# Performance work log

Hardware: AMD Instinct MI355X
Metric: run time of the kernel (lower is better)

## Reference

```python
import jax, jax.numpy as jnp
import numpy as np

N, IN_DIM, HID, OUT = 8192, 512, 256, 64
NEG_INF = -9e15


def setup_inputs() -> dict:
    key = jax.random.key(0)
    ks = jax.random.split(key, 7)
    X = jax.random.normal(ks[0], (N, IN_DIM), dtype=jnp.float32)
    A = jax.random.randint(ks[1], (N, N), 0, 2, dtype=jnp.int32)
    # fc1 (Linear): kaiming-uniform-ish init, exact dist irrelevant for correctness
    W1 = jax.random.normal(ks[2], (IN_DIM, HID), dtype=jnp.float32) / np.sqrt(IN_DIM)
    b1 = jnp.zeros((HID,), dtype=jnp.float32)
    # attention vector a: xavier_uniform(gain=1.414) on shape (2*HID, 1)
    lim = 1.414 * np.sqrt(6.0 / (2 * HID + 1))
    a = jax.random.uniform(ks[3], (2 * HID, 1), minval=-lim, maxval=lim, dtype=jnp.float32)
    Omega = jax.random.normal(ks[4], (HID, OUT), dtype=jnp.float32) * np.sqrt(2.0 / (HID + OUT))
    beta = jnp.zeros((OUT,), dtype=jnp.float32)
    return {"X": X, "A": A, "W1": W1, "b1": b1, "a": a, "Omega": Omega, "beta": beta}


def reference(X, A, W1, b1, a, Omega, beta):
    H1 = X @ W1 + b1                      # [N, HID]
    # score(i,j) = leakyrelu(a[:HID].H1_i + a[HID:].H1_j) -- computed via broadcast,
    # avoiding the O(N^2 * 2*HID) concat the torch code materializes.
    a1 = a[:HID, 0]                       # [HID]
    a2 = a[HID:, 0]                       # [HID]
    e = jax.nn.leaky_relu((H1 @ a1)[:, None] + (H1 @ a2)[None, :], negative_slope=0.2)  # [N, N]
    e = jnp.where(A > 0, e, NEG_INF)
    attention = jax.nn.softmax(e, axis=1)  # dropout_rate=0.0 -> identity
    H2 = attention @ H1                    # [N, HID]
    return jax.nn.sigmoid(H2 @ Omega + beta)  # [N, OUT]
```

## Files before the change

### kernel.cpp

```cpp
#include <hip/hip_runtime.h>
#include <hip/hip_bf16.h>


typedef float f32x4 __attribute__((ext_vector_type(4)));
typedef short s16x8 __attribute__((ext_vector_type(8)));

#define NN 8192
#define INDIM 512
#define HIDD 256
#define OUTD 64

static __device__ __forceinline__ short f2bf(float x) {
    __hip_bfloat16 h = __float2bfloat16(x);
    return __builtin_bit_cast(short, h);
}

static __device__ __forceinline__ void split_bf(float x, short& hi, short& lo) {
    short h = f2bf(x);
    unsigned int hb = ((unsigned int)(unsigned short)h) << 16;
    float hf = __builtin_bit_cast(float, hb);
    hi = h;
    lo = f2bf(x - hf);
}

__global__ void k_splitW1(const float* __restrict__ W1,
                          short* __restrict__ W1Thi, short* __restrict__ W1Tlo) {
    int t = blockIdx.x * 256 + threadIdx.x;
    int n = t >> 9;
    int k = t & 511;
    float x = W1[k * 256 + n];
    short hi, lo; split_bf(x, hi, lo);
    W1Thi[t] = hi;
    W1Tlo[t] = lo;
}

__global__ void __launch_bounds__(256, 2)
k_h1(const float* __restrict__ X, const short* __restrict__ W1Thi,
     const short* __restrict__ W1Tlo, const float* __restrict__ b1,
     const float* __restrict__ avec, unsigned short* __restrict__ H1TB,
     float* __restrict__ alw, float* __restrict__ bew, float* __restrict__ uvw) {
    __shared__ float s1p[4][16];
    __shared__ float s2p[4][16];
    const int tid = threadIdx.x;
    const int wn = tid >> 6, lane = tid & 63;
    const int q = lane >> 4, m16 = lane & 15;
    const int i0 = blockIdx.x * 16;
    const int irow = i0 + m16;

    f32x4 zero4 = {0.f, 0.f, 0.f, 0.f};
    f32x4 acc[4];
#pragma unroll
    for (int nt = 0; nt < 4; ++nt) acc[nt] = zero4;

    const float* Xrow = X + (size_t)irow * INDIM;
    for (int kk = 0; kk < INDIM; kk += 32) {
        const int k0 = kk + q * 8;
        float4 xa = *(const float4*)(Xrow + k0);
        float4 xb = *(const float4*)(Xrow + k0 + 4);
        float xs[8] = {xa.x, xa.y, xa.z, xa.w, xb.x, xb.y, xb.z, xb.w};
        s16x8 ahi, alo;
#pragma unroll
        for (int j = 0; j < 8; ++j) { short h, l; split_bf(xs[j], h, l); ahi[j] = h; alo[j] = l; }
#pragma unroll
        for (int nt = 0; nt < 4; ++nt) {
            const int n = wn * 64 + nt * 16 + m16;
            s16x8 bhi = *(const s16x8*)(W1Thi + n * INDIM + k0);
            s16x8 blo = *(const s16x8*)(W1Tlo + n * INDIM + k0);
            acc[nt] = __builtin_amdgcn_mfma_f32_16x16x32_bf16(ahi, bhi, acc[nt], 0, 0, 0);
            acc[nt] = __builtin_amdgcn_mfma_f32_16x16x32_bf16(ahi, blo, acc[nt], 0, 0, 0);
            acc[nt] = __builtin_amdgcn_mfma_f32_16x16x32_bf16(alo, bhi, acc[nt], 0, 0, 0);
        }
    }

    float p1[4] = {0.f, 0.f, 0.f, 0.f};
    float p2[4] = {0.f, 0.f, 0.f, 0.f};
    const int rowbase = i0 + q * 4;
    const int chunk = rowbase >> 5, win = rowbase & 31;
#pragma unroll
    for (int nt = 0; nt < 4; ++nt) {
        const int col = wn * 64 + nt * 16 + m16;
        const float b1v = b1[col];
        const float a1v = avec[col];
        const float a2v = avec[HIDD + col];
        float v0 = acc[nt][0] + b1v;
        float v1 = acc[nt][1] + b1v;
        float v2 = acc[nt][2] + b1v;
        float v3 = acc[nt][3] + b1v;
        ushort4 us;
        us.x = (unsigned short)f2bf(v0);
        us.y = (unsigned short)f2bf(v1);
        us.z = (unsigned short)f2bf(v2);
        us.w = (unsigned short)f2bf(v3);
        *(ushort4*)(H1TB + (size_t)chunk * 8192 + col * 32 + win) = us;
        p1[0] += v0 * a1v; p1[1] += v1 * a1v; p1[2] += v2 * a1v; p1[3] += v3 * a1v;
        p2[0] += v0 * a2v; p2[1] += v1 * a2v; p2[2] += v2 * a2v; p2[3] += v3 * a2v;
    }
#pragma unroll
    for (int off = 1; off < 16; off <<= 1) {
#pragma unroll
        for (int r = 0; r < 4; ++r) {
            p1[r] += __shfl_xor(p1[r], off);
            p2[r] += __shfl_xor(p2[r], off);
        }
    }
    if (m16 == 0) {
#pragma unroll
        for (int r = 0; r < 4; ++r) {
            s1p[wn][q * 4 + r] = p1[r];
            s2p[wn][q * 4 + r] = p2[r];
        }
    }
    __syncthreads();
    if (tid < 16) {
        const int i = i0 + tid;
        float s1 = s1p[0][tid] + s1p[1][tid] + s1p[2][tid] + s1p[3][tid];
        float s2 = s2p[0][tid] + s2p[1][tid] + s2p[2][tid] + s2p[3][tid];
        alw[i] = expf(s1);
        bew[i] = expf(0.2f * s1);
        uvw[2 * i]     = expf(s2);
        uvw[2 * i + 1] = expf(0.2f * s2);
    }
}

__global__ void __launch_bounds__(256, 4)
k_attn(const int* __restrict__ A, const unsigned short* __restrict__ H1TB,
       const float* __restrict__ alw, const float* __restrict__ bew,
       const float* __restrict__ uvw,
       float* __restrict__ H2acc, float* __restrict__ Zw) {
    __shared__ unsigned short tile[8192];

    const int tid = threadIdx.x;
    const int wave = tid >> 6, lane = tid & 63;
    const int q = lane >> 4, m16 = lane & 15;
    const int wm = wave & 1, wn = wave >> 1;
    const int mb = blockIdx.x & 255;
    const int ks = blockIdx.x >> 8;
    const int i = mb * 32 + wm * 16 + m16;
    const float al = alw[i], be = bew[i];

    const unsigned short* gp = H1TB + (size_t)ks * 64 * 8192 + tid * 8;
    __attribute__((address_space(3))) unsigned short* tl =
        (__attribute__((address_space(3))) unsigned short*)tile;

    const int* Ap = A + (size_t)i * NN + ks * 2048 + q * 8;
    const float* uvp = uvw + 2 * (ks * 2048 + q * 8);

    f32x4 zero4 = {0.f, 0.f, 0.f, 0.f};
    f32x4 acc[8];
#pragma unroll
    for (int nt = 0; nt < 8; ++nt) acc[nt] = zero4;
    float zacc = 0.f;

    for (int kk = 0; kk < 2048; kk += 32) {
#pragma unroll
        for (int c = 0; c < 4; ++c)
            __builtin_amdgcn_global_load_lds(
                (const __attribute__((address_space(1))) void*)(gp + c * 2048),
                (__attribute__((address_space(3))) void*)(tl + c * 2048 + tid * 8),
                16, 0, 0);
        gp += 8192;

        int4 A0 = *(const int4*)(Ap);
        int4 A1 = *(const int4*)(Ap + 4);
        float4 uv0 = *(const float4*)(uvp);
        float4 uv1 = *(const float4*)(uvp + 4);
        float4 uv2 = *(const float4*)(uvp + 8);
        float4 uv3 = *(const float4*)(uvp + 12);
        Ap += 32; uvp += 64;

        float wv[8];
        wv[0] = (A0.x > 0) ? fmaxf(al * uv0.x, be * uv0.y) : 0.f;
        wv[1] = (A0.y > 0) ? fmaxf(al * uv0.z, be * uv0.w) : 0.f;
        wv[2] = (A0.z > 0) ? fmaxf(al * uv1.x, be * uv1.y) : 0.f;
        wv[3] = (A0.w > 0) ? fmaxf(al * uv1.z, be * uv1.w) : 0.f;
        wv[4] = (A1.x > 0) ? fmaxf(al * uv2.x, be * uv2.y) : 0.f;
        wv[5] = (A1.y > 0) ? fmaxf(al * uv2.z, be * uv2.w) : 0.f;
        wv[6] = (A1.z > 0) ? fmaxf(al * uv3.x, be * uv3.y) : 0.f;
        wv[7] = (A1.w > 0) ? fmaxf(al * uv3.z, be * uv3.w) : 0.f;
        zacc += (wv[0] + wv[1] + wv[2] + wv[3]) + (wv[4] + wv[5] + wv[6] + wv[7]);
        s16x8 af;
#pragma unroll
        for (int j = 0; j < 8; ++j) af[j] = f2bf(wv[j]);

        __syncthreads();
#pragma unroll
        for (int nt = 0; nt < 8; ++nt) {
            s16x8 bf = *(const s16x8*)(tile + (wn * 128 + nt * 16 + m16) * 32 + q * 8);
            acc[nt] = __builtin_amdgcn_mfma_f32_16x16x32_bf16(af, bf, acc[nt], 0, 0, 0);
        }
        __syncthreads();
    }

    zacc += __shfl_xor(zacc, 16);
    zacc += __shfl_xor(zacc, 32);
    if (wn == 0 && q == 0) atomicAdd(&Zw[i], zacc);

    const int rowbase = mb * 32 + wm * 16 + q * 4;
#pragma unroll
    for (int nt = 0; nt < 8; ++nt) {
        const int col = wn * 128 + nt * 16 + m16;
#pragma unroll
        for (int r = 0; r < 4; ++r)
            atomicAdd(&H2acc[(size_t)(rowbase + r) * HIDD + col], acc[nt][r]);
    }
}

__global__ void __launch_bounds__(256)
k_out(const float* __restrict__ H2acc, const float* __restrict__ Zw,
      const float* __restrict__ Omega, const float* __restrict__ beta,
      float* __restrict__ out) {
    __shared__ float om[HIDD * OUTD];
    const int tid = threadIdx.x;
    for (int idx = tid; idx < HIDD * OUTD; idx += 256) om[idx] = Omega[idx];
    __syncthreads();
    const int wave = tid >> 6, o = tid & 63;
    const float bv = beta[o];
    for (int rr = 0; rr < 8; ++rr) {
        const int i = blockIdx.x * 32 + wave * 8 + rr;
        const float4* H2v = (const float4*)(H2acc + (size_t)i * HIDD);
        float acc = 0.f;
#pragma unroll 4
        for (int c4 = 0; c4 < 64; ++c4) {
            float4 h = H2v[c4];
            const int cb = c4 * 4;
            acc = fmaf(h.x, om[(cb + 0) * OUTD + o], acc);
            acc = fmaf(h.y, om[(cb + 1) * OUTD + o], acc);
            acc = fmaf(h.z, om[(cb + 2) * OUTD + o], acc);
            acc = fmaf(h.w, om[(cb + 3) * OUTD + o], acc);
        }
        const float zinv = 1.0f / Zw[i];
        const float logit = acc * zinv + bv;
        out[(size_t)i * OUTD + o] = 1.0f / (1.0f + expf(-logit));
    }
}

extern "C" void kernel_launch(void* const* d_in, const int* in_sizes, int n_in,
                              void* d_out, int out_size, void* d_ws, size_t ws_size,
                              hipStream_t stream) {
    const float* X     = (const float*)d_in[0];
    const int*   A     = (const int*)d_in[1];
    const float* W1    = (const float*)d_in[2];
    const float* b1    = (const float*)d_in[3];
    const float* avec  = (const float*)d_in[4];
    const float* Omega = (const float*)d_in[5];
    const float* beta  = (const float*)d_in[6];
    float* out = (float*)d_out;

    char* ws = (char*)d_ws;
    unsigned short* H1TB = (unsigned short*)(ws + 0);
    short* W1Thi = (short*)(ws + 4194304);
    short* W1Tlo = (short*)(ws + 4456448);
    float* alw   = (float*)(ws + 4718592);
    float* bew   = (float*)(ws + 4751360);
    float* uvw   = (float*)(ws + 4784128);
    float* Zw    = (float*)(ws + 4849664);
    float* H2acc = (float*)(ws + 4882432);

    hipMemsetAsync(Zw, 0, 32768 + 8388608, stream);

    k_splitW1<<<512, 256, 0, stream>>>(W1, W1Thi, W1Tlo);
    k_h1<<<512, 256, 0, stream>>>(X, W1Thi, W1Tlo, b1, avec, H1TB, alw, bew, uvw);
    k_attn<<<1024, 256, 0, stream>>>(A, H1TB, alw, bew, uvw, H2acc, Zw);
    k_out<<<256, 256, 0, stream>>>(H2acc, Zw, Omega, beta, out);
}
```

Measured before the change: 545.1 us.

## Double-buffer the H1 LDS tile and prefetch next A/uv loads in attention kernel

Result: slower. 562.0 us (+3.1%).

```diff
diff --git a/kernel.cpp b/kernel.cpp
--- a/kernel.cpp
+++ b/kernel.cpp
@@ -127,7 +127,7 @@
        const float* __restrict__ alw, const float* __restrict__ bew,
        const float* __restrict__ uvw,
        float* __restrict__ H2acc, float* __restrict__ Zw) {
-    __shared__ unsigned short tile[8192];
+    __shared__ unsigned short tile[2][8192];
 
     const int tid = threadIdx.x;
     const int wave = tid >> 6, lane = tid & 63;
@@ -140,7 +140,7 @@
 
     const unsigned short* gp = H1TB + (size_t)ks * 64 * 8192 + tid * 8;
     __attribute__((address_space(3))) unsigned short* tl =
-        (__attribute__((address_space(3))) unsigned short*)tile;
+        (__attribute__((address_space(3))) unsigned short*)&tile[0][0];
 
     const int* Ap = A + (size_t)i * NN + ks * 2048 + q * 8;
     const float* uvp = uvw + 2 * (ks * 2048 + q * 8);
@@ -151,23 +151,23 @@
     for (int nt = 0; nt < 8; ++nt) acc[nt] = zero4;
     float zacc = 0.f;
 
-    for (int kk = 0; kk < 2048; kk += 32) {
-#pragma unroll
-        for (int c = 0; c < 4; ++c)
-            __builtin_amdgcn_global_load_lds(
-                (const __attribute__((address_space(1))) void*)(gp + c * 2048),
-                (__attribute__((address_space(3))) void*)(tl + c * 2048 + tid * 8),
-                16, 0, 0);
-        gp += 8192;
-
-        int4 A0 = *(const int4*)(Ap);
-        int4 A1 = *(const int4*)(Ap + 4);
-        float4 uv0 = *(const float4*)(uvp);
-        float4 uv1 = *(const float4*)(uvp + 4);
-        float4 uv2 = *(const float4*)(uvp + 8);
-        float4 uv3 = *(const float4*)(uvp + 12);
-        Ap += 32; uvp += 64;
-
+#pragma unroll
+    for (int c = 0; c < 4; ++c)
+        __builtin_amdgcn_global_load_lds(
+            (const __attribute__((address_space(1))) void*)(gp + c * 2048),
+            (__attribute__((address_space(3))) void*)(tl + c * 2048 + tid * 8),
+            16, 0, 0);
+    gp += 8192;
+
+    int4 A0 = *(const int4*)(Ap);
+    int4 A1 = *(const int4*)(Ap + 4);
+    float4 uv0 = *(const float4*)(uvp);
+    float4 uv1 = *(const float4*)(uvp + 4);
+    float4 uv2 = *(const float4*)(uvp + 8);
+    float4 uv3 = *(const float4*)(uvp + 12);
+    Ap += 32; uvp += 64;
+
+    for (int kk = 0; kk < 64; ++kk) {
         float wv[8];
         wv[0] = (A0.x > 0) ? fmaxf(al * uv0.x, be * uv0.y) : 0.f;
         wv[1] = (A0.y > 0) ? fmaxf(al * uv0.z, be * uv0.w) : 0.f;
@@ -182,13 +182,35 @@
 #pragma unroll
         for (int j = 0; j < 8; ++j) af[j] = f2bf(wv[j]);
 
-        __syncthreads();
+        __builtin_amdgcn_sched_barrier(0);
+        asm volatile("s_waitcnt vmcnt(0)" ::: "memory");
+        __builtin_amdgcn_s_barrier();
+        __builtin_amdgcn_sched_barrier(0);
+
+        if (kk < 63) {
+            A0 = *(const int4*)(Ap);
+            A1 = *(const int4*)(Ap + 4);
+            uv0 = *(const float4*)(uvp);
+            uv1 = *(const float4*)(uvp + 4);
+            uv2 = *(const float4*)(uvp + 8);
+            uv3 = *(const float4*)(uvp + 12);
+            Ap += 32; uvp += 64;
+            const int nb = ((kk + 1) & 1) * 8192;
+#pragma unroll
+            for (int c = 0; c < 4; ++c)
+                __builtin_amdgcn_global_load_lds(
+                    (const __attribute__((address_space(1))) void*)(gp + c * 2048),
+                    (__attribute__((address_space(3))) void*)(tl + nb + c * 2048 + tid * 8),
+                    16, 0, 0);
+            gp += 8192;
+        }
+
+        const unsigned short* tb = &tile[kk & 1][0];
 #pragma unroll
         for (int nt = 0; nt < 8; ++nt) {
-            s16x8 bf = *(const s16x8*)(tile + (wn * 128 + nt * 16 + m16) * 32 + q * 8);
-            acc[nt] = __builtin_amdgcn_mfma_f32_16x16x32_bf16(af, bf, acc[nt], 0, 0, 0);
-        }
-        __syncthreads();
+            s16x8 bfv = *(const s16x8*)(tb + (wn * 128 + nt * 16 + m16) * 32 + q * 8);
+            acc[nt] = __builtin_amdgcn_mfma_f32_16x16x32_bf16(af, bfv, acc[nt], 0, 0, 0);
+        }
     }
 
     zacc += __shfl_xor(zacc, 16);
```

## Bit-pack adjacency in fused H1 kernel and register-pipeline attention without LDS

Applied to the files above, without the earlier changes.

After: 604.2 us. +10.8%, slower.

```diff
diff --git a/kernel.cpp b/kernel.cpp
--- a/kernel.cpp
+++ b/kernel.cpp
@@ -34,17 +34,58 @@
     W1Tlo[t] = lo;
 }
 
-__global__ void __launch_bounds__(256, 2)
-k_h1(const float* __restrict__ X, const short* __restrict__ W1Thi,
-     const short* __restrict__ W1Tlo, const float* __restrict__ b1,
-     const float* __restrict__ avec, unsigned short* __restrict__ H1TB,
-     float* __restrict__ alw, float* __restrict__ bew, float* __restrict__ uvw) {
+__global__ void __launch_bounds__(256)
+k_fat(const float* __restrict__ X, const short* __restrict__ W1Thi,
+      const short* __restrict__ W1Tlo, const float* __restrict__ b1,
+      const float* __restrict__ avec, unsigned short* __restrict__ H1TB,
+      float* __restrict__ alw, float* __restrict__ bew, float* __restrict__ uvw,
+      const int* __restrict__ A, unsigned int* __restrict__ Apk,
+      float* __restrict__ Zw) {
     __shared__ float s1p[4][16];
     __shared__ float s2p[4][16];
+    const int b = blockIdx.x;
     const int tid = threadIdx.x;
+
+    if (b >= 2560) {
+        f32x4 z4 = {0.f, 0.f, 0.f, 0.f};
+        f32x4* dst = (f32x4*)Zw + (size_t)(b - 2560) * 4112;
+        for (int t = tid; t < 4112; t += 256) dst[t] = z4;
+        return;
+    }
+
+    if (b >= 512) {
+        const int i0 = (b - 512) * 4;
+        const int ks = tid >> 6, q = (tid >> 4) & 3, kk0 = tid & 15;
+#pragma unroll
+        for (int r = 0; r < 4; ++r) {
+            const int i = i0 + r;
+            const int* Ar = A + (size_t)i * NN;
+            unsigned int out = 0;
+#pragma unroll
+            for (int kkq = 0; kkq < 4; ++kkq) {
+                const int kk = kk0 * 4 + kkq;
+                const int c0 = ks * 2048 + kk * 32 + q * 8;
+                int4 v0 = *(const int4*)(Ar + c0);
+                int4 v1 = *(const int4*)(Ar + c0 + 4);
+                unsigned int bb = 0;
+                bb |= (v0.x > 0) ? 1u : 0u;
+                bb |= (v0.y > 0) ? 2u : 0u;
+                bb |= (v0.z > 0) ? 4u : 0u;
+                bb |= (v0.w > 0) ? 8u : 0u;
+                bb |= (v1.x > 0) ? 16u : 0u;
+                bb |= (v1.y > 0) ? 32u : 0u;
+                bb |= (v1.z > 0) ? 64u : 0u;
+                bb |= (v1.w > 0) ? 128u : 0u;
+                out |= bb << (kkq * 8);
+            }
+            Apk[(size_t)i * 256 + tid] = out;
+        }
+        return;
+    }
+
     const int wn = tid >> 6, lane = tid & 63;
     const int q = lane >> 4, m16 = lane & 15;
-    const int i0 = blockIdx.x * 16;
+    const int i0 = b * 16;
     const int irow = i0 + m16;
 
     f32x4 zero4 = {0.f, 0.f, 0.f, 0.f};
@@ -123,85 +164,117 @@
 }
 
 __global__ void __launch_bounds__(256, 4)
-k_attn(const int* __restrict__ A, const unsigned short* __restrict__ H1TB,
+k_attn(const unsigned int* __restrict__ Apk, const unsigned short* __restrict__ H1TB,
        const float* __restrict__ alw, const float* __restrict__ bew,
        const float* __restrict__ uvw,
        float* __restrict__ H2acc, float* __restrict__ Zw) {
-    __shared__ unsigned short tile[8192];
-
     const int tid = threadIdx.x;
-    const int wave = tid >> 6, lane = tid & 63;
+    const int wn = tid >> 6, lane = tid & 63;
     const int q = lane >> 4, m16 = lane & 15;
-    const int wm = wave & 1, wn = wave >> 1;
-    const int mb = blockIdx.x & 255;
-    const int ks = blockIdx.x >> 8;
-    const int i = mb * 32 + wm * 16 + m16;
-    const float al = alw[i], be = bew[i];
-
-    const unsigned short* gp = H1TB + (size_t)ks * 64 * 8192 + tid * 8;
-    __attribute__((address_space(3))) unsigned short* tl =
-        (__attribute__((address_space(3))) unsigned short*)tile;
-
-    const int* Ap = A + (size_t)i * NN + ks * 2048 + q * 8;
+    const int ks = blockIdx.x & 3;
+    const int mb = blockIdx.x >> 2;
+    const int i0 = mb * 32 + m16;
+    const int i1 = i0 + 16;
+    const float al0 = alw[i0], be0 = bew[i0];
+    const float al1 = alw[i1], be1 = bew[i1];
+
+    const size_t hslice = (size_t)ks * 64 * 8192;
+    const int lbase = (wn * 64 + m16) * 32 + q * 8;
+    const unsigned int* Ab0 = Apk + (size_t)i0 * 256 + ks * 64 + q * 16;
+    const unsigned int* Ab1 = Apk + (size_t)i1 * 256 + ks * 64 + q * 16;
     const float* uvp = uvw + 2 * (ks * 2048 + q * 8);
 
     f32x4 zero4 = {0.f, 0.f, 0.f, 0.f};
-    f32x4 acc[8];
-#pragma unroll
-    for (int nt = 0; nt < 8; ++nt) acc[nt] = zero4;
-    float zacc = 0.f;
-
-    for (int kk = 0; kk < 2048; kk += 32) {
-#pragma unroll
-        for (int c = 0; c < 4; ++c)
-            __builtin_amdgcn_global_load_lds(
-                (const __attribute__((address_space(1))) void*)(gp + c * 2048),
-                (__attribute__((address_space(3))) void*)(tl + c * 2048 + tid * 8),
-                16, 0, 0);
-        gp += 8192;
-
-        int4 A0 = *(const int4*)(Ap);
-        int4 A1 = *(const int4*)(Ap + 4);
-        float4 uv0 = *(const float4*)(uvp);
-        float4 uv1 = *(const float4*)(uvp + 4);
-        float4 uv2 = *(const float4*)(uvp + 8);
-        float4 uv3 = *(const float4*)(uvp + 12);
-        Ap += 32; uvp += 64;
-
-        float wv[8];
-        wv[0] = (A0.x > 0) ? fmaxf(al * uv0.x, be * uv0.y) : 0.f;
-        wv[1] = (A0.y > 0) ? fmaxf(al * uv0.z, be * uv0.w) : 0.f;
-        wv[2] = (A0.z > 0) ? fmaxf(al * uv1.x, be * uv1.y) : 0.f;
-        wv[3] = (A0.w > 0) ? fmaxf(al * uv1.z, be * uv1.w) : 0.f;
-        wv[4] = (A1.x > 0) ? fmaxf(al * uv2.x, be * uv2.y) : 0.f;
-        wv[5] = (A1.y > 0) ? fmaxf(al * uv2.z, be * uv2.w) : 0.f;
-        wv[6] = (A1.z > 0) ? fmaxf(al * uv3.x, be * uv3.y) : 0.f;
-        wv[7] = (A1.w > 0) ? fmaxf(al * uv3.z, be * uv3.w) : 0.f;
-        zacc += (wv[0] + wv[1] + wv[2] + wv[3]) + (wv[4] + wv[5] + wv[6] + wv[7]);
-        s16x8 af;
-#pragma unroll
-        for (int j = 0; j < 8; ++j) af[j] = f2bf(wv[j]);
-
-        __syncthreads();
-#pragma unroll
-        for (int nt = 0; nt < 8; ++nt) {
-            s16x8 bf = *(const s16x8*)(tile + (wn * 128 + nt * 16 + m16) * 32 + q * 8);
-            acc[nt] = __builtin_amdgcn_mfma_f32_16x16x32_bf16(af, bf, acc[nt], 0, 0, 0);
-        }
-        __syncthreads();
-    }
-
-    zacc += __shfl_xor(zacc, 16);
-    zacc += __shfl_xor(zacc, 32);
-    if (wn == 0 && q == 0) atomicAdd(&Zw[i], zacc);
-
-    const int rowbase = mb * 32 + wm * 16 + q * 4;
-#pragma unroll
-    for (int nt = 0; nt < 8; ++nt) {
-        const int col = wn * 128 + nt * 16 + m16;
-#pragma unroll
-        for (int r = 0; r < 4; ++r)
-            atomicAdd(&H2acc[(size_t)(rowbase + r) * HIDD + col], acc[nt][r]);
+    f32x4 acc0[4], acc1[4];
+#pragma unroll
+    for (int nt = 0; nt < 4; ++nt) { acc0[nt] = zero4; acc1[nt] = zero4; }
+    float zacc0 = 0.f, zacc1 = 0.f;
+
+    s16x8 bA[4], bB[4];
+#pragma unroll
+    for (int nt = 0; nt < 4; ++nt)
+        bA[nt] = *(const s16x8*)(H1TB + hslice + lbase + nt * 512);
+    float4 uv0 = *(const float4*)(uvp);
+    float4 uv1 = *(const float4*)(uvp + 4);
+    float4 uv2 = *(const float4*)(uvp + 8);
+    float4 uv3 = *(const float4*)(uvp + 12);
+    uvp += 64;
+    unsigned int a40 = Ab0[0], a41 = Ab1[0];
+
+#define STEP(BC, BN, KK, KKQ)                                                          \
+    {                                                                                  \
+        const unsigned int ab0 = a40 >> ((KKQ) * 8);                                   \
+        const unsigned int ab1 = a41 >> ((KKQ) * 8);                                   \
+        float w0[8], w1[8];                                                            \
+        w0[0] = (ab0 & 1u)   ? fmaxf(al0 * uv0.x, be0 * uv0.y) : 0.f;                  \
+        w0[1] = (ab0 & 2u)   ? fmaxf(al0 * uv0.z, be0 * uv0.w) : 0.f;                  \
+        w0[2] = (ab0 & 4u)   ? fmaxf(al0 * uv1.x, be0 * uv1.y) : 0.f;                  \
+        w0[3] = (ab0 & 8u)   ? fmaxf(al0 * uv1.z, be0 * uv1.w) : 0.f;                  \
+        w0[4] = (ab0 & 16u)  ? fmaxf(al0 * uv2.x, be0 * uv2.y) : 0.f;                  \
+        w0[5] = (ab0 & 32u)  ? fmaxf(al0 * uv2.z, be0 * uv2.w) : 0.f;                  \
+        w0[6] = (ab0 & 64u)  ? fmaxf(al0 * uv3.x, be0 * uv3.y) : 0.f;                  \
+        w0[7] = (ab0 & 128u) ? fmaxf(al0 * uv3.z, be0 * uv3.w) : 0.f;                  \
+        w1[0] = (ab1 & 1u)   ? fmaxf(al1 * uv0.x, be1 * uv0.y) : 0.f;                  \
+        w1[1] = (ab1 & 2u)   ? fmaxf(al1 * uv0.z, be1 * uv0.w) : 0.f;                  \
+        w1[2] = (ab1 & 4u)   ? fmaxf(al1 * uv1.x, be1 * uv1.y) : 0.f;                  \
+        w1[3] = (ab1 & 8u)   ? fmaxf(al1 * uv1.z, be1 * uv1.w) : 0.f;                  \
+        w1[4] = (ab1 & 16u)  ? fmaxf(al1 * uv2.x, be1 * uv2.y) : 0.f;                  \
+        w1[5] = (ab1 & 32u)  ? fmaxf(al1 * uv2.z, be1 * uv2.w) : 0.f;                  \
+        w1[6] = (ab1 & 64u)  ? fmaxf(al1 * uv3.x, be1 * uv3.y) : 0.f;                  \
+        w1[7] = (ab1 & 128u) ? fmaxf(al1 * uv3.z, be1 * uv3.w) : 0.f;                  \
+        zacc0 += (w0[0] + w0[1] + w0[2] + w0[3]) + (w0[4] + w0[5] + w0[6] + w0[7]);    \
+        zacc1 += (w1[0] + w1[1] + w1[2] + w1[3]) + (w1[4] + w1[5] + w1[6] + w1[7]);    \
+        s16x8 af0, af1;                                                                \
+        _Pragma("unroll")                                                              \
+        for (int j = 0; j < 8; ++j) { af0[j] = f2bf(w0[j]); af1[j] = f2bf(w1[j]); }    \
+        uv0 = *(const float4*)(uvp);                                                   \
+        uv1 = *(const float4*)(uvp + 4);                                               \
+        uv2 = *(const float4*)(uvp + 8);                                               \
+        uv3 = *(const float4*)(uvp + 12);                                              \
+        uvp += 64;                                                                     \
+        {                                                                              \
+            const unsigned short* hq = H1TB + hslice + (size_t)((KK) + 1) * 8192 + lbase; \
+            _Pragma("unroll")                                                          \
+            for (int nt = 0; nt < 4; ++nt) BN[nt] = *(const s16x8*)(hq + nt * 512);    \
+        }                                                                              \
+        _Pragma("unroll")                                                              \
+        for (int nt = 0; nt < 4; ++nt) {                                               \
+            acc0[nt] = __builtin_amdgcn_mfma_f32_16x16x32_bf16(af0, BC[nt], acc0[nt], 0, 0, 0); \
+            acc1[nt] = __builtin_amdgcn_mfma_f32_16x16x32_bf16(af1, BC[nt], acc1[nt], 0, 0, 0); \
+        }                                                                              \
+    }
+
+    for (int kk4 = 0; kk4 < 16; ++kk4) {
+        const unsigned int a40n = Ab0[(kk4 + 1) & 15];
+        const unsigned int a41n = Ab1[(kk4 + 1) & 15];
+        const int kb = kk4 * 4;
+        STEP(bA, bB, kb + 0, 0)
+        STEP(bB, bA, kb + 1, 1)
+        STEP(bA, bB, kb + 2, 2)
+        STEP(bB, bA, kb + 3, 3)
+        a40 = a40n;
+        a41 = a41n;
+    }
+#undef STEP
+
+    zacc0 += __shfl_xor(zacc0, 16);
+    zacc0 += __shfl_xor(zacc0, 32);
+    zacc1 += __shfl_xor(zacc1, 16);
+    zacc1 += __shfl_xor(zacc1, 32);
+    if (wn == 0 && q == 0) {
+        atomicAdd(&Zw[i0], zacc0);
+        atomicAdd(&Zw[i1], zacc1);
+    }
+
+    const int r0 = mb * 32 + q * 4;
+#pragma unroll
+    for (int nt = 0; nt < 4; ++nt) {
+        const int col = wn * 64 + nt * 16 + m16;
+#pragma unroll
+        for (int r = 0; r < 4; ++r) {
+            atomicAdd(&H2acc[(size_t)(r0 + r) * HIDD + col], acc0[nt][r]);
+            atomicAdd(&H2acc[(size_t)(r0 + 16 + r) * HIDD + col], acc1[nt][r]);
+        }
     }
 }
 
@@ -255,11 +328,11 @@
     float* uvw   = (float*)(ws + 4784128);
     float* Zw    = (float*)(ws + 4849664);
     float* H2acc = (float*)(ws + 4882432);
-
-    hipMemsetAsync(Zw, 0, 32768 + 8388608, stream);
+    unsigned int* Apk = (unsigned int*)(ws + 13271040);
 
     k_splitW1<<<512, 256, 0, stream>>>(W1, W1Thi, W1Tlo);
-    k_h1<<<512, 256, 0, stream>>>(X, W1Thi, W1Tlo, b1, avec, H1TB, alw, bew, uvw);
-    k_attn<<<1024, 256, 0, stream>>>(A, H1TB, alw, bew, uvw, H2acc, Zw);
+    k_fat<<<2688, 256, 0, stream>>>(X, W1Thi, W1Tlo, b1, avec, H1TB, alw, bew, uvw,
+                                    A, Apk, Zw);
+    k_attn<<<1024, 256, 0, stream>>>(Apk, H1TB, alw, bew, uvw, H2acc, Zw);
     k_out<<<256, 256, 0, stream>>>(H2acc, Zw, Omega, beta, out);
 }
```
